# Kernel optimization log

Hardware: AMD Instinct MI355X
Metric: run time of the kernel (lower is better)

Reference implementation:

```python
import jax, jax.numpy as jnp
import numpy as np

B, C, N = 4, 512, 4096
CQK = C // 8

def setup_inputs() -> dict:
    key = jax.random.key(0)
    ks = jax.random.split(key, 8)
    s = 0.02  # weight init scale
    return {
        "x": jax.random.normal(ks[0], (B, C, N), dtype=jnp.float32),
        "Wq": jax.random.normal(ks[1], (CQK, C), dtype=jnp.float32) * s,
        "bq": jax.random.normal(ks[2], (CQK,), dtype=jnp.float32) * s,
        "Wk": jax.random.normal(ks[3], (CQK, C), dtype=jnp.float32) * s,
        "bk": jax.random.normal(ks[4], (CQK,), dtype=jnp.float32) * s,
        "Wv": jax.random.normal(ks[5], (C, C), dtype=jnp.float32) * s,
        "bv": jax.random.normal(ks[6], (C,), dtype=jnp.float32) * s,
        "gamma": jax.random.normal(ks[7], (1,), dtype=jnp.float32),
    }

def reference(x, Wq, bq, Wk, bk, Wv, bv, gamma):
    # pointwise Conv1d == per-point matmul: [B,C,N] -> [B,Cout,N]
    q = jnp.einsum('oc,bcn->bon', Wq, x) + bq[None, :, None]   # [B,CQK,N]
    k = jnp.einsum('oc,bcn->bon', Wk, x) + bk[None, :, None]   # [B,CQK,N]
    v = jnp.einsum('oc,bcn->bon', Wv, x) + bv[None, :, None]   # [B,C,N]
    # attention[b,i,j] = sum_c q[b,c,i] * k[b,c,j]  (unscaled, non-causal)
    attn = jnp.einsum('bci,bcj->bij', q, k)                    # [B,N,N]
    attn = jax.nn.softmax(attn, axis=-1)
    # out[b,c,i] = sum_j v[b,c,j] * attn[b,i,j]
    out = jnp.einsum('bcj,bij->bci', v, attn)                  # [B,C,N]
    return gamma[0] * out + x
```

## Files before the change

### kernel.cpp

```cpp
#include <hip/hip_runtime.h>
#include <math.h>

#define B_ 4
#define C_ 512
#define N_ 4096
#define LOG2E 1.44269504088896f

typedef __attribute__((ext_vector_type(8))) short s8v;
typedef __attribute__((ext_vector_type(4))) float f4v;

#define MF32(a, b, c) __builtin_amdgcn_mfma_f32_16x16x32_bf16(a, b, c, 0, 0, 0)

#if defined(__has_builtin) && __has_builtin(__builtin_amdgcn_exp2f)
#define EXP2(x) __builtin_amdgcn_exp2f(x)
#else
#define EXP2(x) exp2f(x)
#endif

#define BARRIER_LDS() do {                                   \
    __builtin_amdgcn_sched_barrier(0);                       \
    asm volatile("s_waitcnt lgkmcnt(0)" ::: "memory");       \
    __builtin_amdgcn_s_barrier();                            \
    __builtin_amdgcn_sched_barrier(0);                       \
} while (0)

static __device__ __forceinline__ ushort f2bf(float f) {
    unsigned u = __float_as_uint(f);
    u += 0x7FFFu + ((u >> 16) & 1u);
    return (ushort)(u >> 16);
}
static __device__ __forceinline__ unsigned pack2bf(float a, float b) {
    unsigned ua = __float_as_uint(a); ua += 0x7FFFu + ((ua >> 16) & 1u);
    unsigned ub = __float_as_uint(b); ub += 0x7FFFu + ((ub >> 16) & 1u);
    return (ua >> 16) | (ub & 0xffff0000u);
}

__global__ __launch_bounds__(256) void wconv_kernel(
    const float* __restrict__ Wq, const float* __restrict__ Wk,
    const float* __restrict__ Wv, ushort* __restrict__ Wb)
{
    const int row = blockIdx.x;
    const float* src = row < 64 ? Wq + (size_t)row * C_
                     : row < 128 ? Wk + (size_t)(row - 64) * C_
                     : Wv + (size_t)(row - 128) * C_;
    const int t2 = threadIdx.x * 2;
    float2 v = *(const float2*)&src[t2];
    ushort2 o; o.x = f2bf(v.x); o.y = f2bf(v.y);
    *(ushort2*)&Wb[(size_t)row * C_ + t2] = o;
}

__global__ __launch_bounds__(512, 2) void qkv_fused(
    const float* __restrict__ x, const ushort* __restrict__ Wb,
    const float* __restrict__ bq, const float* __restrict__ bk,
    const float* __restrict__ bv,
    ushort* __restrict__ qT, ushort* __restrict__ kT, ushort* __restrict__ vB)
{
    __shared__ ushort Xs[32 * 544];

    const int tid = threadIdx.x, w = tid >> 6, lane = tid & 63;
    const int li = lane & 15, qd = lane >> 4;
    const int n0 = blockIdx.x * 32, b = blockIdx.y;

    {
        const int cg = tid >> 3;
        const int ch = tid & 7;
        #pragma unroll
        for (int r = 0; r < 8; ++r) {
            const int c = r * 64 + cg;
            float4 v = *(const float4*)&x[((size_t)b * C_ + c) * N_ + n0 + ch * 4];
            Xs[(ch * 4 + 0) * 544 + c] = f2bf(v.x);
            Xs[(ch * 4 + 1) * 544 + c] = f2bf(v.y);
            Xs[(ch * 4 + 2) * 544 + c] = f2bf(v.z);
            Xs[(ch * 4 + 3) * 544 + c] = f2bf(v.w);
        }
    }
    __syncthreads();

    const int rb0 = w * 80;
    f4v acc[5][2];
    #pragma unroll
    for (int ot = 0; ot < 5; ++ot)
        #pragma unroll
        for (int nt = 0; nt < 2; ++nt)
            acc[ot][nt] = (f4v){0.f, 0.f, 0.f, 0.f};

    #pragma unroll 2
    for (int kc = 0; kc < C_; kc += 32) {
        s8v aw[5], bx[2];
        #pragma unroll
        for (int ot = 0; ot < 5; ++ot)
            aw[ot] = *(const s8v*)&Wb[(size_t)(rb0 + ot * 16 + li) * C_ + kc + qd * 8];
        #pragma unroll
        for (int nt = 0; nt < 2; ++nt)
            bx[nt] = *(const s8v*)&Xs[(nt * 16 + li) * 544 + kc + qd * 8];
        #pragma unroll
        for (int ot = 0; ot < 5; ++ot) {
            if (rb0 + ot * 16 >= 128) {
                #pragma unroll
                for (int nt = 0; nt < 2; ++nt)
                    acc[ot][nt] = MF32(bx[nt], aw[ot], acc[ot][nt]);
            } else {
                #pragma unroll
                for (int nt = 0; nt < 2; ++nt)
                    acc[ot][nt] = MF32(aw[ot], bx[nt], acc[ot][nt]);
            }
        }
    }

    #pragma unroll
    for (int ot = 0; ot < 5; ++ot) {
        const int rb = rb0 + ot * 16;
        if (rb < 128) {
            ushort* dst = rb < 64 ? qT : kT;
            const float* bias = rb < 64 ? bq : bk;
            const int ob = (rb < 64 ? rb : rb - 64) + qd * 4;
            const float sc = rb < 64 ? LOG2E : 1.0f;
            #pragma unroll
            for (int nt = 0; nt < 2; ++nt) {
                const int n = n0 + nt * 16 + li;
                ushort4 o;
                o.x = f2bf((acc[ot][nt][0] + bias[ob + 0]) * sc);
                o.y = f2bf((acc[ot][nt][1] + bias[ob + 1]) * sc);
                o.z = f2bf((acc[ot][nt][2] + bias[ob + 2]) * sc);
                o.w = f2bf((acc[ot][nt][3] + bias[ob + 3]) * sc);
                *(ushort4*)&dst[((size_t)b * N_ + n) * 64 + ob] = o;
            }
        } else {
            const int c = rb - 128 + li;
            const float bb = bv[c];
            #pragma unroll
            for (int nt = 0; nt < 2; ++nt) {
                const int n = n0 + nt * 16 + qd * 4;
                ushort4 o;
                o.x = f2bf(acc[ot][nt][0] + bb);
                o.y = f2bf(acc[ot][nt][1] + bb);
                o.z = f2bf(acc[ot][nt][2] + bb);
                o.w = f2bf(acc[ot][nt][3] + bb);
                *(ushort4*)&vB[((size_t)b * C_ + c) * N_ + n] = o;
            }
        }
    }
}

__device__ __forceinline__ void pv_chunk(
    const ushort* __restrict__ Pr, int li, int qd, int cidx,
    const s8v* vf, f4v (&acc)[2][8])
{
    #pragma unroll
    for (int h = 0; h < 2; ++h) {
        s8v pf[4];
        #pragma unroll
        for (int g = 0; g < 4; ++g)
            pf[g] = *(const s8v*)&Pr[(size_t)((h * 4 + g) * 16 + li) * 136 + cidx * 32 + qd * 8];
        #pragma unroll
        for (int ct = 0; ct < 2; ++ct)
            #pragma unroll
            for (int g = 0; g < 4; ++g)
                acc[ct][h * 4 + g] = MF32(vf[ct], pf[g], acc[ct][h * 4 + g]);
    }
}

__device__ __forceinline__ void s_phase(
    s8v ck0, s8v ck1, const s8v (&qf)[8][2], float (&lp)[8],
    ushort* __restrict__ Pw, int li, int qd, int w)
{
    #pragma unroll
    for (int h = 0; h < 2; ++h) {
        f4v sac[4];
        #pragma unroll
        for (int g = 0; g < 4; ++g) {
            const int it = h * 4 + g;
            sac[g] = (f4v){0.f, 0.f, 0.f, 0.f};
            sac[g] = MF32(ck0, qf[it][0], sac[g]);
            sac[g] = MF32(ck1, qf[it][1], sac[g]);
        }
        #pragma unroll
        for (int g = 0; g < 4; ++g) {
            const int it = h * 4 + g;
            const float p0 = EXP2(sac[g][0]);
            const float p1 = EXP2(sac[g][1]);
            const float p2 = EXP2(sac[g][2]);
            const float p3 = EXP2(sac[g][3]);
            lp[it] += (p0 + p1) + (p2 + p3);
            uint2 u; u.x = pack2bf(p0, p1); u.y = pack2bf(p2, p3);
            *(uint2*)&Pw[(size_t)(it * 16 + li) * 136 + w * 16 + qd * 4] = u;
        }
    }
}

__global__ __launch_bounds__(512, 2) void attn_mfma(
    const ushort* __restrict__ qT, const ushort* __restrict__ kT,
    const ushort* __restrict__ vB, const float* __restrict__ x,
    const float* __restrict__ gamma, float* __restrict__ out)
{
    extern __shared__ char smem[];
    ushort* Pb0 = (ushort*)smem;
    ushort* Pb1 = (ushort*)(smem + 34816);
    float*  l_s = (float*)(smem + 69632);

    const int tid = threadIdx.x, w = tid >> 6, lane = tid & 63;
    const int li = lane & 15, qd = lane >> 4;
    const int i_base = blockIdx.x * 128;
    const int c_base = blockIdx.y * 256;
    const int b = blockIdx.z;

    const ushort* qTb = qT + (size_t)b * N_ * 64;
    const ushort* kTb = kT + (size_t)b * N_ * 64;
    const ushort* vBb = vB + (size_t)b * C_ * N_;

    s8v qf[8][2];
    #pragma unroll
    for (int it = 0; it < 8; ++it)
        #pragma unroll
        for (int ks = 0; ks < 2; ++ks)
            qf[it][ks] = *(const s8v*)&qTb[(size_t)(i_base + it * 16 + li) * 64 + ks * 32 + qd * 8];

    f4v acc[2][8];
    #pragma unroll
    for (int ct = 0; ct < 2; ++ct)
        #pragma unroll
        for (int it = 0; it < 8; ++it)
            acc[ct][it] = (f4v){0.f, 0.f, 0.f, 0.f};
    float lp[8] = {0.f, 0.f, 0.f, 0.f, 0.f, 0.f, 0.f, 0.f};

    const ushort* kptr = kTb + (size_t)(w * 16 + li) * 64 + qd * 8;
    const ushort* vptr[2];
    #pragma unroll
    for (int ct = 0; ct < 2; ++ct)
        vptr[ct] = vBb + (size_t)(c_base + w * 32 + ct * 16 + li) * N_ + qd * 8;

    s8v kc0 = *(const s8v*)(kptr);
    s8v kc1 = *(const s8v*)(kptr + 32);
    s8v vcur[4];
    #pragma unroll
    for (int ch = 0; ch < 2; ++ch)
        #pragma unroll
        for (int ct = 0; ct < 2; ++ct)
            vcur[ch * 2 + ct] = *(const s8v*)(vptr[ct] + ch * 32);

    s8v kn0 = *(const s8v*)(kptr + (size_t)128 * 64);
    s8v kn1 = *(const s8v*)(kptr + (size_t)128 * 64 + 32);

    s_phase(kc0, kc1, qf, lp, Pb0, li, qd, w);
    BARRIER_LDS();

    #pragma unroll 1
    for (int t = 1; t < N_ / 128; ++t) {
        const ushort* Pr = ((t - 1) & 1) ? Pb1 : Pb0;
        ushort*       Pw = ((t - 1) & 1) ? Pb0 : Pb1;
        const size_t jprev = (size_t)(t - 1) * 128;
        const size_t jcur  = (size_t)t * 128;
        const size_t jnext = (t + 1 < N_ / 128) ? jcur + 128 : 0;

        s8v ck0 = kn0, ck1 = kn1;
        kn0 = *(const s8v*)(kptr + jnext * 64);
        kn1 = *(const s8v*)(kptr + jnext * 64 + 32);

        s8v vlt0[2], vlt1[2], vnx[4];
        #pragma unroll
        for (int ct = 0; ct < 2; ++ct)
            vlt0[ct] = *(const s8v*)(vptr[ct] + jprev + 2 * 32);
        pv_chunk(Pr, li, qd, 0, &vcur[0], acc);
        #pragma unroll
        for (int ct = 0; ct < 2; ++ct)
            vlt1[ct] = *(const s8v*)(vptr[ct] + jprev + 3 * 32);
        pv_chunk(Pr, li, qd, 1, &vcur[2], acc);
        #pragma unroll
        for (int ct = 0; ct < 2; ++ct)
            vnx[ct] = *(const s8v*)(vptr[ct] + jcur);
        pv_chunk(Pr, li, qd, 2, vlt0, acc);
        #pragma unroll
        for (int ct = 0; ct < 2; ++ct)
            vnx[2 + ct] = *(const s8v*)(vptr[ct] + jcur + 32);
        pv_chunk(Pr, li, qd, 3, vlt1, acc);

        s_phase(ck0, ck1, qf, lp, Pw, li, qd, w);

        #pragma unroll
        for (int k = 0; k < 4; ++k) vcur[k] = vnx[k];
        BARRIER_LDS();
    }

    {
        const ushort* Pr = ((N_ / 128 - 1) & 1) ? Pb1 : Pb0;
        const size_t jprev = (size_t)(N_ / 128 - 1) * 128;
        s8v vlt0[2], vlt1[2];
        #pragma unroll
        for (int ct = 0; ct < 2; ++ct)
            vlt0[ct] = *(const s8v*)(vptr[ct] + jprev + 2 * 32);
        pv_chunk(Pr, li, qd, 0, &vcur[0], acc);
        #pragma unroll
        for (int ct = 0; ct < 2; ++ct)
            vlt1[ct] = *(const s8v*)(vptr[ct] + jprev + 3 * 32);
        pv_chunk(Pr, li, qd, 1, &vcur[2], acc);
        pv_chunk(Pr, li, qd, 2, vlt0, acc);
        pv_chunk(Pr, li, qd, 3, vlt1, acc);
    }

    #pragma unroll
    for (int it = 0; it < 8; ++it) {
        lp[it] += __shfl_xor(lp[it], 16, 64);
        lp[it] += __shfl_xor(lp[it], 32, 64);
    }
    if (qd == 0) {
        #pragma unroll
        for (int it = 0; it < 8; ++it) l_s[w * 128 + it * 16 + li] = lp[it];
    }
    __syncthreads();
    float inv[8];
    #pragma unroll
    for (int it = 0; it < 8; ++it) {
        float t = 0.f;
        #pragma unroll
        for (int ww = 0; ww < 8; ++ww) t += l_s[ww * 128 + it * 16 + li];
        inv[it] = 1.0f / t;
    }

    const float g = gamma[0];
    #pragma unroll
    for (int ct = 0; ct < 2; ++ct)
        #pragma unroll
        for (int it = 0; it < 8; ++it) {
            const int i = i_base + it * 16 + li;
            #pragma unroll
            for (int r = 0; r < 4; ++r) {
                const int c = c_base + w * 32 + ct * 16 + qd * 4 + r;
                const size_t off = ((size_t)b * C_ + c) * N_ + i;
                out[off] = g * acc[ct][it][r] * inv[it] + x[off];
            }
        }
}

extern "C" void kernel_launch(void* const* d_in, const int* in_sizes, int n_in,
                              void* d_out, int out_size, void* d_ws, size_t ws_size,
                              hipStream_t stream)
{
    const float* x     = (const float*)d_in[0];
    const float* Wq    = (const float*)d_in[1];
    const float* bq    = (const float*)d_in[2];
    const float* Wk    = (const float*)d_in[3];
    const float* bk    = (const float*)d_in[4];
    const float* Wv    = (const float*)d_in[5];
    const float* bv    = (const float*)d_in[6];
    const float* gamma = (const float*)d_in[7];
    float* out = (float*)d_out;

    ushort* vB = (ushort*)d_ws;
    ushort* qT = vB + (size_t)B_ * C_ * N_;
    ushort* kT = qT + (size_t)B_ * N_ * 64;
    ushort* Wb = kT + (size_t)B_ * N_ * 64;

    wconv_kernel<<<dim3(640), 256, 0, stream>>>(Wq, Wk, Wv, Wb);
    qkv_fused<<<dim3(N_ / 32, B_), 512, 0, stream>>>(x, Wb, bq, bk, bv, qT, kT, vB);
    attn_mfma<<<dim3(N_ / 128, 2, B_), 512, 73728, stream>>>(qT, kT, vB, x, gamma, out);
}
```

Baseline: 234.9 us.

## Widen QKV projection tile to 64 points with swizzled LDS and prefetched weights

The QKV projection kernel now handles 64 points per block instead of 32, which doubles reuse of each weight fragment loaded from global memory across four MFMA column tiles. The padded LDS layout is replaced by an XOR-swizzled 64KB dynamic shared buffer to avoid bank conflicts. Weight fragments for the next k-chunk are prefetched into registers during the current step. The cost is higher register and LDS use, which lowers occupancy, and half as many blocks, which may underfill the GPU.

```diff
diff --git a/kernel.cpp b/kernel.cpp
--- a/kernel.cpp
+++ b/kernel.cpp
@@ -55,56 +55,72 @@
     const float* __restrict__ bv,
     ushort* __restrict__ qT, ushort* __restrict__ kT, ushort* __restrict__ vB)
 {
-    __shared__ ushort Xs[32 * 544];
+    extern __shared__ ushort Xs[];
 
     const int tid = threadIdx.x, w = tid >> 6, lane = tid & 63;
     const int li = lane & 15, qd = lane >> 4;
-    const int n0 = blockIdx.x * 32, b = blockIdx.y;
-
-    {
-        const int cg = tid >> 3;
-        const int ch = tid & 7;
-        #pragma unroll
-        for (int r = 0; r < 8; ++r) {
-            const int c = r * 64 + cg;
-            float4 v = *(const float4*)&x[((size_t)b * C_ + c) * N_ + n0 + ch * 4];
-            Xs[(ch * 4 + 0) * 544 + c] = f2bf(v.x);
-            Xs[(ch * 4 + 1) * 544 + c] = f2bf(v.y);
-            Xs[(ch * 4 + 2) * 544 + c] = f2bf(v.z);
-            Xs[(ch * 4 + 3) * 544 + c] = f2bf(v.w);
-        }
+    const int n0 = blockIdx.x * 64, b = blockIdx.y;
+
+    #pragma unroll
+    for (int r = 0; r < 16; ++r) {
+        const int f = r * 512 + tid;
+        const int c = f >> 4;
+        const int nch = f & 15;
+        float4 v = *(const float4*)&x[((size_t)b * C_ + c) * N_ + n0 + nch * 4];
+        const int n = nch * 4;
+        Xs[((n + 0) * 512 + c) ^ (((n + 0) & 7) << 3)] = f2bf(v.x);
+        Xs[((n + 1) * 512 + c) ^ (((n + 1) & 7) << 3)] = f2bf(v.y);
+        Xs[((n + 2) * 512 + c) ^ (((n + 2) & 7) << 3)] = f2bf(v.z);
+        Xs[((n + 3) * 512 + c) ^ (((n + 3) & 7) << 3)] = f2bf(v.w);
     }
     __syncthreads();
 
     const int rb0 = w * 80;
-    f4v acc[5][2];
+    const ushort* wrow[5];
     #pragma unroll
     for (int ot = 0; ot < 5; ++ot)
-        #pragma unroll
-        for (int nt = 0; nt < 2; ++nt)
+        wrow[ot] = Wb + (size_t)(rb0 + ot * 16 + li) * C_ + qd * 8;
+
+    f4v acc[5][4];
+    #pragma unroll
+    for (int ot = 0; ot < 5; ++ot)
+        #pragma unroll
+        for (int nt = 0; nt < 4; ++nt)
             acc[ot][nt] = (f4v){0.f, 0.f, 0.f, 0.f};
 
-    #pragma unroll 2
+    s8v awc[5], awn[5];
+    #pragma unroll
+    for (int ot = 0; ot < 5; ++ot)
+        awc[ot] = *(const s8v*)(wrow[ot]);
+
+    #pragma unroll 1
     for (int kc = 0; kc < C_; kc += 32) {
-        s8v aw[5], bx[2];
+        const int kn = (kc + 32 < C_) ? kc + 32 : 0;
         #pragma unroll
         for (int ot = 0; ot < 5; ++ot)
-            aw[ot] = *(const s8v*)&Wb[(size_t)(rb0 + ot * 16 + li) * C_ + kc + qd * 8];
-        #pragma unroll
-        for (int nt = 0; nt < 2; ++nt)
-            bx[nt] = *(const s8v*)&Xs[(nt * 16 + li) * 544 + kc + qd * 8];
+            awn[ot] = *(const s8v*)(wrow[ot] + kn);
+
+        s8v bx[4];
+        #pragma unroll
+        for (int nt = 0; nt < 4; ++nt) {
+            const int n = nt * 16 + li;
+            bx[nt] = *(const s8v*)&Xs[((n * 512) + kc + qd * 8) ^ ((li & 7) << 3)];
+        }
+
         #pragma unroll
         for (int ot = 0; ot < 5; ++ot) {
             if (rb0 + ot * 16 >= 128) {
                 #pragma unroll
-                for (int nt = 0; nt < 2; ++nt)
-                    acc[ot][nt] = MF32(bx[nt], aw[ot], acc[ot][nt]);
+                for (int nt = 0; nt < 4; ++nt)
+                    acc[ot][nt] = MF32(bx[nt], awc[ot], acc[ot][nt]);
             } else {
                 #pragma unroll
-                for (int nt = 0; nt < 2; ++nt)
-                    acc[ot][nt] = MF32(aw[ot], bx[nt], acc[ot][nt]);
+                for (int nt = 0; nt < 4; ++nt)
+                    acc[ot][nt] = MF32(awc[ot], bx[nt], acc[ot][nt]);
             }
         }
+        #pragma unroll
+        for (int ot = 0; ot < 5; ++ot) awc[ot] = awn[ot];
     }
 
     #pragma unroll
@@ -116,7 +132,7 @@
             const int ob = (rb < 64 ? rb : rb - 64) + qd * 4;
             const float sc = rb < 64 ? LOG2E : 1.0f;
             #pragma unroll
-            for (int nt = 0; nt < 2; ++nt) {
+            for (int nt = 0; nt < 4; ++nt) {
                 const int n = n0 + nt * 16 + li;
                 ushort4 o;
                 o.x = f2bf((acc[ot][nt][0] + bias[ob + 0]) * sc);
@@ -129,7 +145,7 @@
             const int c = rb - 128 + li;
             const float bb = bv[c];
             #pragma unroll
-            for (int nt = 0; nt < 2; ++nt) {
+            for (int nt = 0; nt < 4; ++nt) {
                 const int n = n0 + nt * 16 + qd * 4;
                 ushort4 o;
                 o.x = f2bf(acc[ot][nt][0] + bb);
@@ -351,6 +367,6 @@
     ushort* Wb = kT + (size_t)B_ * N_ * 64;
 
     wconv_kernel<<<dim3(640), 256, 0, stream>>>(Wq, Wk, Wv, Wb);
-    qkv_fused<<<dim3(N_ / 32, B_), 512, 0, stream>>>(x, Wb, bq, bk, bv, qT, kT, vB);
+    qkv_fused<<<dim3(N_ / 64, B_), 512, 65536, stream>>>(x, Wb, bq, bk, bv, qT, kT, vB);
     attn_mfma<<<dim3(N_ / 128, 2, B_), 512, 73728, stream>>>(qT, kT, vB, x, gamma, out);
 }
```

Measured after the change: 223.2 us. 1.05x faster.
